# Performance work log

Measured on AMD Instinct MI355X. Metric: run time of the kernel, lower is better.

## Reference

```python
import jax, jax.numpy as jnp
import numpy as np

ALPHA = 3.0   # self.alpha
TAU = 0.1     # contrastive temperature
K = 8         # configs.k (top-k hyperedges per node)


def _scale(x, w, ehy, enod):
    """One scale of incidence_matrix_learn.
    x: [B, L, D] series tokens; w: [ws, D] word tokens;
    ehy: [H, D] hyperedge embedding table; enod: [N, D] node embedding table, N = L + ws.
    Returns (binary incidence matrix [N, H] float32, scalar contrastive loss).
    """
    B = x.shape[0]
    # concat_all[i]: cat(x.permute(0,2,1), word_expanded) -> [B, D, N]
    we = jnp.broadcast_to(w.T[None], (B,) + w.T.shape)          # [B, D, ws]
    concat = jnp.concatenate([jnp.transpose(x, (0, 2, 1)), we], axis=-1)  # [B, D, N]
    N, H = enod.shape[0], ehy.shape[0]
    # adjacency: softmax(relu(alpha * nodeec @ hyperen.T)) along hyperedge dim
    a = enod @ ehy.T                                            # [N, H]
    adj = jax.nn.softmax(jax.nn.relu(ALPHA * a), axis=-1)
    # top-k mask + threshold > 0.5 -> binary incidence matrix
    k = min(H, K)
    _, idx = jax.lax.top_k(adj, k)                              # [N, k]
    mask = jnp.zeros_like(adj).at[jnp.arange(N)[:, None], idx].set(1.0)
    adj_bin = ((adj * mask) > 0.5).astype(jnp.float32)          # [N, H]
    # positives: nodes sharing any hyperedge (build_pos_indices_from_edge_index),
    # equivalent to (A A^T > 0) with self excluded; dropping all-zero columns is a no-op here
    P = (adj_bin @ adj_bin.T > 0) & ~jnp.eye(N, dtype=bool)     # [N, N]
    cnt = P.sum(axis=1)                                         # positives per node
    # acl_loss_batched, vectorized over batch and nodes
    nodes = jnp.transpose(concat, (0, 2, 1))                    # [B, N, D]
    nrm = nodes / jnp.maximum(jnp.linalg.norm(nodes, axis=-1, keepdims=True), 1e-12)
    sim = jnp.einsum('bnd,bmd->bnm', nrm, nrm) / TAU            # [B, N, N]
    denom = jax.nn.logsumexp(sim, axis=-1)                      # [B, N]
    pos_mean = jnp.einsum('bnm,nm->bn', sim, P.astype(sim.dtype)) / jnp.maximum(cnt, 1)
    valid = cnt > 0                                             # [N]
    loss_sum = jnp.sum(jnp.where(valid[None, :], denom - pos_mean, 0.0))
    vc = B * valid.sum()
    loss = jnp.where(vc > 0, loss_sum / jnp.maximum(vc, 1), 0.0)
    return adj_bin, loss


def setup_inputs() -> dict:
    key = jax.random.key(0)
    ks = jax.random.split(key, 8)
    B, D = 64, 512
    return dict(
        x0=jax.random.normal(ks[0], (B, 512, D), dtype=jnp.float32),
        x1=jax.random.normal(ks[1], (B, 256, D), dtype=jnp.float32),
        word0=jax.random.normal(ks[2], (128, D), dtype=jnp.float32),
        word1=jax.random.normal(ks[3], (128, D), dtype=jnp.float32),
        embhy0=jax.random.normal(ks[4], (128, D), dtype=jnp.float32),
        embhy1=jax.random.normal(ks[5], (64, D), dtype=jnp.float32),
        embnod0=jax.random.normal(ks[6], (640, D), dtype=jnp.float32),
        embnod1=jax.random.normal(ks[7], (384, D), dtype=jnp.float32),
    )


def reference(x0, x1, word0, word1, embhy0, embhy1, embnod0, embnod1):
    a0, l0 = _scale(x0, word0, embhy0, embnod0)
    a1, l1 = _scale(x1, word1, embhy1, embnod1)
    return (a0, a1, l0 + l1)
```

## Files before the change

### kernel.cpp

```cpp
#include <hip/hip_runtime.h>


#define DDIM 512
#define BATCH 64
#define NGID 65536

typedef __attribute__((ext_vector_type(8))) short short8;
typedef __attribute__((ext_vector_type(4))) float f32x4;

__device__ __forceinline__ unsigned short f2bf(float f) {
  unsigned int u = __float_as_uint(f);
  u += 0x7fffu + ((u >> 16) & 1u);
  return (unsigned short)(u >> 16);
}

__device__ __forceinline__ void async16(const void* g, void* l) {
  __builtin_amdgcn_global_load_lds(
      (const __attribute__((address_space(1))) unsigned int*)g,
      (__attribute__((address_space(3))) unsigned int*)l, 16, 0, 0);
}

__device__ __forceinline__ int m3(int x) {
  x -= (x >= 6) ? 6 : 0;
  x -= (x >= 3) ? 3 : 0;
  return x;
}

__global__ __launch_bounds__(256) void prep_adj(
    const float* __restrict__ enod0, const float* __restrict__ ehy0,
    const float* __restrict__ enod1, const float* __restrict__ ehy1,
    float* __restrict__ adj0, float* __restrict__ adj1,
    int* __restrict__ labels0, int* __restrict__ labels1,
    float* __restrict__ acc) {
  const int t = threadIdx.x;
  if (blockIdx.x == 0 && t == 0) { acc[0] = 0.f; acc[1] = 0.f; }
  const bool s0 = blockIdx.x < 640;
  const int n = s0 ? blockIdx.x : blockIdx.x - 640;
  const int H = s0 ? 128 : 64;
  const float* enod = s0 ? enod0 : enod1;
  const float* ehy = s0 ? ehy0 : ehy1;
  float* out_adj = s0 ? adj0 : adj1;
  int* labels = s0 ? labels0 : labels1;
  __shared__ float erow[DDIM];
  __shared__ float red[128];
  __shared__ int lab;
  if (t < 128) ((float4*)erow)[t] = ((const float4*)(enod + (size_t)n * DDIM))[t];
  if (t == 0) lab = -1;
  __syncthreads();
  float v = 0.f;
  if (t < H) {
    const float4* hr = (const float4*)(ehy + (size_t)t * DDIM);
    float a = 0.f;
    #pragma unroll 8
    for (int d = 0; d < DDIM / 4; ++d) {
      float4 h = hr[d];
      float4 e = ((const float4*)erow)[d];
      a = fmaf(h.x, e.x, a); a = fmaf(h.y, e.y, a);
      a = fmaf(h.z, e.z, a); a = fmaf(h.w, e.w, a);
    }
    v = fmaxf(0.f, 3.0f * a);
  }
  if (t < 128) red[t] = v;
  __syncthreads();
  for (int s = 64; s > 0; s >>= 1) {
    if (t < s) red[t] = fmaxf(red[t], red[t + s]);
    __syncthreads();
  }
  const float mx = red[0];
  __syncthreads();
  const float e = (t < H) ? __expf(v - mx) : 0.f;
  if (t < 128) red[t] = e;
  __syncthreads();
  for (int s = 64; s > 0; s >>= 1) {
    if (t < s) red[t] += red[t + s];
    __syncthreads();
  }
  const float sum = red[0];
  if (t < H) {
    const float adj = e / sum;
    const float bin = (adj > 0.5f) ? 1.0f : 0.0f;
    out_adj[(size_t)n * H + t] = bin;
    if (bin > 0.f) lab = t;
  }
  __syncthreads();
  if (t == 0) labels[n] = lab;
}

__global__ __launch_bounds__(256) void prep_norm(
    const float* __restrict__ x0, const float* __restrict__ w0,
    const float* __restrict__ x1, const float* __restrict__ w1,
    unsigned short* __restrict__ nhat0, unsigned short* __restrict__ nhat1) {
  const int t = threadIdx.x;
  const int wave = t >> 6;
  const int lane = t & 63;
  const int g = blockIdx.x * 4 + wave;
  const bool s0 = g < BATCH * 640;
  const int gg = s0 ? g : g - BATCH * 640;
  const int N = s0 ? 640 : 384;
  const int L = s0 ? 512 : 256;
  const float* x = s0 ? x0 : x1;
  const float* w = s0 ? w0 : w1;
  unsigned short* nhat = s0 ? nhat0 : nhat1;
  const int b = gg / N;
  const int n = gg - b * N;
  const float* src = (n < L) ? (x + ((size_t)b * L + n) * DDIM)
                             : (w + (size_t)(n - L) * DDIM);
  const float4* rowp = (const float4*)src;
  const float4 v0 = rowp[lane];
  const float4 v1 = rowp[lane + 64];
  float ss = v0.x * v0.x + v0.y * v0.y + v0.z * v0.z + v0.w * v0.w +
             v1.x * v1.x + v1.y * v1.y + v1.z * v1.z + v1.w * v1.w;
  #pragma unroll
  for (int off = 32; off > 0; off >>= 1) ss += __shfl_xor(ss, off);
  const float rinv = 1.0f / fmaxf(sqrtf(ss), 1e-12f);
  ushort4 o0, o1;
  o0.x = f2bf(v0.x * rinv); o0.y = f2bf(v0.y * rinv);
  o0.z = f2bf(v0.z * rinv); o0.w = f2bf(v0.w * rinv);
  o1.x = f2bf(v1.x * rinv); o1.y = f2bf(v1.y * rinv);
  o1.z = f2bf(v1.z * rinv); o1.w = f2bf(v1.w * rinv);
  ushort4* op = (ushort4*)(nhat + ((size_t)b * N + n) * DDIM);
  op[lane] = o0;
  op[lane + 64] = o1;
}

__global__ __launch_bounds__(256) void cnt_kernel(
    const int* __restrict__ labels0, int* __restrict__ cnt0,
    const int* __restrict__ labels1, int* __restrict__ cnt1,
    int* __restrict__ valid) {
  const bool s0 = blockIdx.x == 0;
  const int* labels = s0 ? labels0 : labels1;
  int* cnt = s0 ? cnt0 : cnt1;
  int* validcnt = s0 ? valid : valid + 1;
  const int N = s0 ? 640 : 384;
  __shared__ int lab[640];
  __shared__ int hist[128];
  __shared__ int vc;
  const int t = threadIdx.x;
  if (t == 0) vc = 0;
  if (t < 128) hist[t] = 0;
  for (int i = t; i < N; i += 256) lab[i] = labels[i];
  __syncthreads();
  for (int i = t; i < N; i += 256)
    if (lab[i] >= 0) atomicAdd(&hist[lab[i]], 1);
  __syncthreads();
  int lv = 0;
  for (int i = t; i < N; i += 256) {
    const int c = (lab[i] >= 0) ? hist[lab[i]] - 1 : 0;
    cnt[i] = c;
    if (c > 0) ++lv;
  }
  if (lv > 0) atomicAdd(&vc, lv);
  __syncthreads();
  if (t == 0) *validcnt = vc;
}

__global__ __launch_bounds__(128, 2) void lse_kernel(
    const unsigned short* __restrict__ nhat0, const int* __restrict__ labels0,
    const unsigned short* __restrict__ nhat1, const int* __restrict__ labels1,
    float2* __restrict__ sp) {
  __shared__ short8 Bbuf[3][512];
  __shared__ float2 redC[2][64];
  __shared__ int labS[640];
  const int tid = threadIdx.x;
  const bool s0 = blockIdx.x < 640;
  const int i = s0 ? blockIdx.x : blockIdx.x - 640;
  const int tu = i >> 6;
  const int b = i & 63;
  const int nt = s0 ? 10 : 6;
  const int N = s0 ? 640 : 384;
  const unsigned short* nhat = s0 ? nhat0 : nhat1;
  const int* labels = s0 ? labels0 : labels1;
  const int gbase = s0 ? b * 640 : 40960 + b * 384;

  const int wave = tid >> 6;
  const int lane = tid & 63;
  const int lrow = lane & 15;
  const int lq = lane >> 4;

  for (int t = tid; t < N; t += 128) labS[t] = labels[t];

  const size_t base = (size_t)b * N * DDIM;
  const int rw0 = tu * 64 + wave * 32;
  const unsigned short* Ap0 = nhat + base + (size_t)(rw0 + lrow) * DDIM + lq * 8;
  const unsigned short* Ap1 = Ap0 + (size_t)16 * DDIM;
  short8 a0[16], a1[16];
  #pragma unroll
  for (int ks = 0; ks < 16; ++ks) {
    a0[ks] = *(const short8*)(Ap0 + ks * 32);
    a1[ks] = *(const short8*)(Ap1 + ks * 32);
  }
  #pragma unroll
  for (int ks = 0; ks < 16; ++ks)
    asm volatile("" :: "v"(a0[ks]), "v"(a1[ks]));

  __syncthreads();

  int labn[2][4];
  #pragma unroll
  for (int s = 0; s < 2; ++s)
    #pragma unroll
    for (int r = 0; r < 4; ++r) labn[s][r] = labS[rw0 + s * 16 + lq * 4 + r];

  const unsigned short* Bp0 = nhat + base + (size_t)tu * 64 * DDIM;
  const int f0 = wave * 4;
  #pragma unroll
  for (int pc = 0; pc < 2; ++pc) {
    #pragma unroll
    for (int fi = 0; fi < 4; ++fi) {
      const int f = f0 + fi, j = f >> 1, ks = f & 1;
      async16(Bp0 + (size_t)(j * 16 + lrow) * DDIM + pc * 64 + ks * 32 + lq * 8,
              &Bbuf[pc][f * 64]);
    }
  }

  float rSE[2][4] = {{0.f, 0.f, 0.f, 0.f}, {0.f, 0.f, 0.f, 0.f}};
  float rPOS[2][4] = {{0.f, 0.f, 0.f, 0.f}, {0.f, 0.f, 0.f, 0.f}};
  int slotb = 0;

  for (int tv = tu; tv < nt; ++tv) {
    const bool diag = (tv == tu);
    const bool last = (tv == nt - 1);
    const unsigned short* Bcur = nhat + base + (size_t)tv * 64 * DDIM;
    const unsigned short* Bnxt = Bcur + (size_t)64 * DDIM;
    const int sl[3] = {slotb, m3(slotb + 1), m3(slotb + 2)};

    f32x4 acc[4][2];
    #pragma unroll
    for (int j = 0; j < 4; ++j) {
      acc[j][0] = (f32x4){0.f, 0.f, 0.f, 0.f};
      acc[j][1] = (f32x4){0.f, 0.f, 0.f, 0.f};
    }
    #pragma unroll
    for (int kc = 0; kc < 8; ++kc) {
      if (last && kc == 7) asm volatile("s_waitcnt vmcnt(0)" ::: "memory");
      else                 asm volatile("s_waitcnt vmcnt(4)" ::: "memory");
      __builtin_amdgcn_s_barrier();
      if (!(last && kc >= 6)) {
        const unsigned short* Bsrc = (kc < 6) ? Bcur : Bnxt;
        const int kcol = (kc < 6) ? kc + 2 : kc - 6;
        short8* dst = &Bbuf[sl[(kc + 2) % 3]][0];
        #pragma unroll
        for (int fi = 0; fi < 4; ++fi) {
          const int f = f0 + fi, j = f >> 1, ks = f & 1;
          async16(Bsrc + (size_t)(j * 16 + lrow) * DDIM + kcol * 64 + ks * 32 + lq * 8,
                  dst + f * 64);
        }
      }
      const short8* bb = &Bbuf[sl[kc % 3]][0];
      #pragma unroll
      for (int ks = 0; ks < 2; ++ks) {
        const short8 b0 = bb[(0 + ks) * 64 + lane];
        const short8 b1 = bb[(2 + ks) * 64 + lane];
        const short8 b2 = bb[(4 + ks) * 64 + lane];
        const short8 b3 = bb[(6 + ks) * 64 + lane];
        const short8 av0 = a0[kc * 2 + ks];
        const short8 av1 = a1[kc * 2 + ks];
        acc[0][0] = __builtin_amdgcn_mfma_f32_16x16x32_bf16(av0, b0, acc[0][0], 0, 0, 0);
        acc[0][1] = __builtin_amdgcn_mfma_f32_16x16x32_bf16(av1, b0, acc[0][1], 0, 0, 0);
        acc[1][0] = __builtin_amdgcn_mfma_f32_16x16x32_bf16(av0, b1, acc[1][0], 0, 0, 0);
        acc[1][1] = __builtin_amdgcn_mfma_f32_16x16x32_bf16(av1, b1, acc[1][1], 0, 0, 0);
        acc[2][0] = __builtin_amdgcn_mfma_f32_16x16x32_bf16(av0, b2, acc[2][0], 0, 0, 0);
        acc[2][1] = __builtin_amdgcn_mfma_f32_16x16x32_bf16(av1, b2, acc[2][1], 0, 0, 0);
        acc[3][0] = __builtin_amdgcn_mfma_f32_16x16x32_bf16(av0, b3, acc[3][0], 0, 0, 0);
        acc[3][1] = __builtin_amdgcn_mfma_f32_16x16x32_bf16(av1, b3, acc[3][1], 0, 0, 0);
      }
    }

    float cSE[4] = {0.f, 0.f, 0.f, 0.f};
    float cPOS[4] = {0.f, 0.f, 0.f, 0.f};
    #pragma unroll
    for (int j = 0; j < 4; ++j) {
      const int v = tv * 64 + j * 16 + lrow;
      const int labm = labS[v];
      #pragma unroll
      for (int s = 0; s < 2; ++s) {
        const int u0 = rw0 + s * 16 + lq * 4;
        #pragma unroll
        for (int r = 0; r < 4; ++r) {
          const float sim = acc[j][s][r] * 10.0f;
          const float e = __expf(sim - 10.0f);
          rSE[s][r] += e;
          const bool match = (labn[s][r] >= 0) && (labm == labn[s][r]);
          if (match && v != u0 + r) rPOS[s][r] += sim;
          if (!diag) {
            cSE[j] += e;
            if (match) cPOS[j] += sim;
          }
        }
      }
    }
    if (!diag) {
      #pragma unroll
      for (int off = 16; off <= 32; off <<= 1) {
        #pragma unroll
        for (int j = 0; j < 4; ++j) {
          cSE[j] += __shfl_xor(cSE[j], off);
          cPOS[j] += __shfl_xor(cPOS[j], off);
        }
      }
      if (lane < 16) {
        #pragma unroll
        for (int j = 0; j < 4; ++j) {
          float2 st; st.x = cSE[j]; st.y = cPOS[j];
          redC[wave][j * 16 + lane] = st;
        }
      }
      asm volatile("s_waitcnt lgkmcnt(0)" ::: "memory");
      __builtin_amdgcn_s_barrier();
      if (lane < 32) {
        const int v = wave * 32 + lane;
        const float2 c0 = redC[0][v];
        const float2 c1 = redC[1][v];
        float2 st; st.x = c0.x + c1.x; st.y = c0.y + c1.y;
        sp[(size_t)(1 + tu) * NGID + gbase + tv * 64 + v] = st;
      }
    }
    slotb = m3(slotb + 2);
  }

  #pragma unroll
  for (int off = 1; off <= 8; off <<= 1) {
    #pragma unroll
    for (int s = 0; s < 2; ++s)
      #pragma unroll
      for (int r = 0; r < 4; ++r) {
        rSE[s][r] += __shfl_xor(rSE[s][r], off);
        rPOS[s][r] += __shfl_xor(rPOS[s][r], off);
      }
  }
  if (lrow == 0) {
    #pragma unroll
    for (int s = 0; s < 2; ++s)
      #pragma unroll
      for (int r = 0; r < 4; ++r) {
        const int u = rw0 + s * 16 + lq * 4 + r;
        float2 st; st.x = rSE[s][r]; st.y = rPOS[s][r];
        sp[gbase + u] = st;
      }
  }
}

__global__ __launch_bounds__(256) void loss_reduce(
    const float2* __restrict__ sp, const int* __restrict__ cnt0,
    const int* __restrict__ cnt1, float* __restrict__ acc) {
  __shared__ float r0[4], r1[4];
  const int t = threadIdx.x;
  float l0 = 0.f, l1 = 0.f;
  for (int g = blockIdx.x * 256 + t; g < NGID; g += 64 * 256) {
    const bool is0 = g < 40960;
    const int n = is0 ? (g % 640) : ((g - 40960) % 384);
    const int tb = n >> 6;
    float se = 0.f, pos = 0.f;
    for (int s = 0; s <= tb; ++s) {
      const float2 v = sp[(size_t)s * NGID + g];
      se += v.x; pos += v.y;
    }
    const int c = is0 ? cnt0[n] : cnt1[n];
    if (c > 0) {
      const float v = (10.0f + logf(se)) - pos / (float)c;
      if (is0) l0 += v; else l1 += v;
    }
  }
  #pragma unroll
  for (int off = 32; off > 0; off >>= 1) {
    l0 += __shfl_xor(l0, off);
    l1 += __shfl_xor(l1, off);
  }
  if ((t & 63) == 0) { r0[t >> 6] = l0; r1[t >> 6] = l1; }
  __syncthreads();
  if (t == 0) {
    atomicAdd(&acc[0], r0[0] + r0[1] + r0[2] + r0[3]);
    atomicAdd(&acc[1], r1[0] + r1[1] + r1[2] + r1[3]);
  }
}

__global__ void final_kernel(const float* __restrict__ acc,
                             const int* __restrict__ valid,
                             float* __restrict__ out) {
  float l = 0.f;
  if (valid[0] > 0) l += acc[0] / (float)(BATCH * valid[0]);
  if (valid[1] > 0) l += acc[1] / (float)(BATCH * valid[1]);
  out[0] = l;
}

extern "C" void kernel_launch(void* const* d_in, const int* in_sizes, int n_in,
                              void* d_out, int out_size, void* d_ws,
                              size_t ws_size, hipStream_t stream) {
  const float* x0 = (const float*)d_in[0];
  const float* x1 = (const float*)d_in[1];
  const float* w0 = (const float*)d_in[2];
  const float* w1 = (const float*)d_in[3];
  const float* ehy0 = (const float*)d_in[4];
  const float* ehy1 = (const float*)d_in[5];
  const float* enod0 = (const float*)d_in[6];
  const float* enod1 = (const float*)d_in[7];

  float* out = (float*)d_out;
  float* adj0 = out;
  float* adj1 = out + 640 * 128;
  float* lossp = out + 640 * 128 + 384 * 64;

  unsigned short* nhat0 = (unsigned short*)d_ws;
  unsigned short* nhat1 = nhat0 + (size_t)BATCH * 640 * DDIM;
  int* ip = (int*)(nhat1 + (size_t)BATCH * 384 * DDIM);
  int* labels0 = ip;
  int* labels1 = labels0 + 640;
  int* cnt0 = labels1 + 384;
  int* cnt1 = cnt0 + 640;
  int* valid = cnt1 + 384;
  float* acc = (float*)(valid + 2);
  float2* sp = (float2*)((((size_t)(acc + 2)) + 255) & ~(size_t)255);

  prep_adj<<<1024, 256, 0, stream>>>(enod0, ehy0, enod1, ehy1, adj0, adj1,
                                     labels0, labels1, acc);
  prep_norm<<<16384, 256, 0, stream>>>(x0, w0, x1, w1, nhat0, nhat1);
  cnt_kernel<<<2, 256, 0, stream>>>(labels0, cnt0, labels1, cnt1, valid);
  lse_kernel<<<1024, 128, 0, stream>>>(nhat0, labels0, nhat1, labels1, sp);
  loss_reduce<<<64, 256, 0, stream>>>(sp, cnt0, cnt1, acc);
  final_kernel<<<1, 1, 0, stream>>>(acc, valid, lossp);
}
```

Measured before the change: 263.0 us.

## Merge prep kernels, fold final into reduce, and rebalance lse block order

Combines the adjacency and normalization prep kernels into one launch, and folds the final loss computation into loss_reduce using a last-block ticket. Block-to-tile mapping in lse_kernel now comes from constant tables that interleave heavy and light triangular work units across scales to balance load. Register pinning of the A fragments moves into the loop. This removes two launches and aims to reduce tail imbalance, at the cost of a ticket atomic and a hand-tuned schedule table.

New measurement: 252.2 us. 1.04x faster.

```diff
diff --git a/kernel.cpp b/kernel.cpp
--- a/kernel.cpp
+++ b/kernel.cpp
@@ -7,6 +7,9 @@
 
 typedef __attribute__((ext_vector_type(8))) short short8;
 typedef __attribute__((ext_vector_type(4))) float f32x4;
+
+__constant__ int POS_SCALE[16] = {0,0,0,0, 0,1,0,0, 1,1,0,0, 0,1,1,1};
+__constant__ int POS_TU[16]    = {0,1,2,3, 9,5,7,4, 0,1,5,6, 8,2,3,4};
 
 __device__ __forceinline__ unsigned short f2bf(float f) {
   unsigned int u = __float_as_uint(f);
@@ -26,101 +29,100 @@
   return x;
 }
 
-__global__ __launch_bounds__(256) void prep_adj(
+__global__ __launch_bounds__(256) void prep_kernel(
     const float* __restrict__ enod0, const float* __restrict__ ehy0,
     const float* __restrict__ enod1, const float* __restrict__ ehy1,
     float* __restrict__ adj0, float* __restrict__ adj1,
     int* __restrict__ labels0, int* __restrict__ labels1,
-    float* __restrict__ acc) {
-  const int t = threadIdx.x;
-  if (blockIdx.x == 0 && t == 0) { acc[0] = 0.f; acc[1] = 0.f; }
-  const bool s0 = blockIdx.x < 640;
-  const int n = s0 ? blockIdx.x : blockIdx.x - 640;
-  const int H = s0 ? 128 : 64;
-  const float* enod = s0 ? enod0 : enod1;
-  const float* ehy = s0 ? ehy0 : ehy1;
-  float* out_adj = s0 ? adj0 : adj1;
-  int* labels = s0 ? labels0 : labels1;
-  __shared__ float erow[DDIM];
-  __shared__ float red[128];
-  __shared__ int lab;
-  if (t < 128) ((float4*)erow)[t] = ((const float4*)(enod + (size_t)n * DDIM))[t];
-  if (t == 0) lab = -1;
-  __syncthreads();
-  float v = 0.f;
-  if (t < H) {
-    const float4* hr = (const float4*)(ehy + (size_t)t * DDIM);
-    float a = 0.f;
-    #pragma unroll 8
-    for (int d = 0; d < DDIM / 4; ++d) {
-      float4 h = hr[d];
-      float4 e = ((const float4*)erow)[d];
-      a = fmaf(h.x, e.x, a); a = fmaf(h.y, e.y, a);
-      a = fmaf(h.z, e.z, a); a = fmaf(h.w, e.w, a);
-    }
-    v = fmaxf(0.f, 3.0f * a);
-  }
-  if (t < 128) red[t] = v;
-  __syncthreads();
-  for (int s = 64; s > 0; s >>= 1) {
-    if (t < s) red[t] = fmaxf(red[t], red[t + s]);
-    __syncthreads();
-  }
-  const float mx = red[0];
-  __syncthreads();
-  const float e = (t < H) ? __expf(v - mx) : 0.f;
-  if (t < 128) red[t] = e;
-  __syncthreads();
-  for (int s = 64; s > 0; s >>= 1) {
-    if (t < s) red[t] += red[t + s];
-    __syncthreads();
-  }
-  const float sum = red[0];
-  if (t < H) {
-    const float adj = e / sum;
-    const float bin = (adj > 0.5f) ? 1.0f : 0.0f;
-    out_adj[(size_t)n * H + t] = bin;
-    if (bin > 0.f) lab = t;
-  }
-  __syncthreads();
-  if (t == 0) labels[n] = lab;
-}
-
-__global__ __launch_bounds__(256) void prep_norm(
     const float* __restrict__ x0, const float* __restrict__ w0,
     const float* __restrict__ x1, const float* __restrict__ w1,
-    unsigned short* __restrict__ nhat0, unsigned short* __restrict__ nhat1) {
+    unsigned short* __restrict__ nhat0, unsigned short* __restrict__ nhat1,
+    float* __restrict__ acc, int* __restrict__ ticket) {
   const int t = threadIdx.x;
-  const int wave = t >> 6;
-  const int lane = t & 63;
-  const int g = blockIdx.x * 4 + wave;
-  const bool s0 = g < BATCH * 640;
-  const int gg = s0 ? g : g - BATCH * 640;
-  const int N = s0 ? 640 : 384;
-  const int L = s0 ? 512 : 256;
-  const float* x = s0 ? x0 : x1;
-  const float* w = s0 ? w0 : w1;
-  unsigned short* nhat = s0 ? nhat0 : nhat1;
-  const int b = gg / N;
-  const int n = gg - b * N;
-  const float* src = (n < L) ? (x + ((size_t)b * L + n) * DDIM)
-                             : (w + (size_t)(n - L) * DDIM);
-  const float4* rowp = (const float4*)src;
-  const float4 v0 = rowp[lane];
-  const float4 v1 = rowp[lane + 64];
-  float ss = v0.x * v0.x + v0.y * v0.y + v0.z * v0.z + v0.w * v0.w +
-             v1.x * v1.x + v1.y * v1.y + v1.z * v1.z + v1.w * v1.w;
-  #pragma unroll
-  for (int off = 32; off > 0; off >>= 1) ss += __shfl_xor(ss, off);
-  const float rinv = 1.0f / fmaxf(sqrtf(ss), 1e-12f);
-  ushort4 o0, o1;
-  o0.x = f2bf(v0.x * rinv); o0.y = f2bf(v0.y * rinv);
-  o0.z = f2bf(v0.z * rinv); o0.w = f2bf(v0.w * rinv);
-  o1.x = f2bf(v1.x * rinv); o1.y = f2bf(v1.y * rinv);
-  o1.z = f2bf(v1.z * rinv); o1.w = f2bf(v1.w * rinv);
-  ushort4* op = (ushort4*)(nhat + ((size_t)b * N + n) * DDIM);
-  op[lane] = o0;
-  op[lane + 64] = o1;
+  if (blockIdx.x < 1024) {
+    if (blockIdx.x == 0 && t == 0) { acc[0] = 0.f; acc[1] = 0.f; ticket[0] = 0; }
+    const bool s0 = blockIdx.x < 640;
+    const int n = s0 ? blockIdx.x : blockIdx.x - 640;
+    const int H = s0 ? 128 : 64;
+    const float* enod = s0 ? enod0 : enod1;
+    const float* ehy = s0 ? ehy0 : ehy1;
+    float* out_adj = s0 ? adj0 : adj1;
+    int* labels = s0 ? labels0 : labels1;
+    __shared__ float erow[DDIM];
+    __shared__ float red[128];
+    __shared__ int lab;
+    if (t < 128) ((float4*)erow)[t] = ((const float4*)(enod + (size_t)n * DDIM))[t];
+    if (t == 0) lab = -1;
+    __syncthreads();
+    float v = 0.f;
+    if (t < H) {
+      const float4* hr = (const float4*)(ehy + (size_t)t * DDIM);
+      float a = 0.f;
+      #pragma unroll 8
+      for (int d = 0; d < DDIM / 4; ++d) {
+        float4 h = hr[d];
+        float4 e = ((const float4*)erow)[d];
+        a = fmaf(h.x, e.x, a); a = fmaf(h.y, e.y, a);
+        a = fmaf(h.z, e.z, a); a = fmaf(h.w, e.w, a);
+      }
+      v = fmaxf(0.f, 3.0f * a);
+    }
+    if (t < 128) red[t] = v;
+    __syncthreads();
+    for (int s = 64; s > 0; s >>= 1) {
+      if (t < s) red[t] = fmaxf(red[t], red[t + s]);
+      __syncthreads();
+    }
+    const float mx = red[0];
+    __syncthreads();
+    const float e = (t < H) ? __expf(v - mx) : 0.f;
+    if (t < 128) red[t] = e;
+    __syncthreads();
+    for (int s = 64; s > 0; s >>= 1) {
+      if (t < s) red[t] += red[t + s];
+      __syncthreads();
+    }
+    const float sum = red[0];
+    if (t < H) {
+      const float adj = e / sum;
+      const float bin = (adj > 0.5f) ? 1.0f : 0.0f;
+      out_adj[(size_t)n * H + t] = bin;
+      if (bin > 0.f) lab = t;
+    }
+    __syncthreads();
+    if (t == 0) labels[n] = lab;
+  } else {
+    const int wave = t >> 6;
+    const int lane = t & 63;
+    const int g = (blockIdx.x - 1024) * 4 + wave;
+    const bool s0 = g < BATCH * 640;
+    const int gg = s0 ? g : g - BATCH * 640;
+    const int N = s0 ? 640 : 384;
+    const int L = s0 ? 512 : 256;
+    const float* x = s0 ? x0 : x1;
+    const float* w = s0 ? w0 : w1;
+    unsigned short* nhat = s0 ? nhat0 : nhat1;
+    const int b = gg / N;
+    const int n = gg - b * N;
+    const float* src = (n < L) ? (x + ((size_t)b * L + n) * DDIM)
+                               : (w + (size_t)(n - L) * DDIM);
+    const float4* rowp = (const float4*)src;
+    const float4 v0 = rowp[lane];
+    const float4 v1 = rowp[lane + 64];
+    float ss = v0.x * v0.x + v0.y * v0.y + v0.z * v0.z + v0.w * v0.w +
+               v1.x * v1.x + v1.y * v1.y + v1.z * v1.z + v1.w * v1.w;
+    #pragma unroll
+    for (int off = 32; off > 0; off >>= 1) ss += __shfl_xor(ss, off);
+    const float rinv = 1.0f / fmaxf(sqrtf(ss), 1e-12f);
+    ushort4 o0, o1;
+    o0.x = f2bf(v0.x * rinv); o0.y = f2bf(v0.y * rinv);
+    o0.z = f2bf(v0.z * rinv); o0.w = f2bf(v0.w * rinv);
+    o1.x = f2bf(v1.x * rinv); o1.y = f2bf(v1.y * rinv);
+    o1.z = f2bf(v1.z * rinv); o1.w = f2bf(v1.w * rinv);
+    ushort4* op = (ushort4*)(nhat + ((size_t)b * N + n) * DDIM);
+    op[lane] = o0;
+    op[lane + 64] = o1;
+  }
 }
 
 __global__ __launch_bounds__(256) void cnt_kernel(
@@ -162,10 +164,10 @@
   __shared__ float2 redC[2][64];
   __shared__ int labS[640];
   const int tid = threadIdx.x;
-  const bool s0 = blockIdx.x < 640;
-  const int i = s0 ? blockIdx.x : blockIdx.x - 640;
-  const int tu = i >> 6;
-  const int b = i & 63;
+  const int pos = blockIdx.x >> 6;
+  const int b = blockIdx.x & 63;
+  const bool s0 = POS_SCALE[pos] == 0;
+  const int tu = POS_TU[pos];
   const int nt = s0 ? 10 : 6;
   const int N = s0 ? 640 : 384;
   const unsigned short* nhat = s0 ? nhat0 : nhat1;
@@ -189,9 +191,6 @@
     a0[ks] = *(const short8*)(Ap0 + ks * 32);
     a1[ks] = *(const short8*)(Ap1 + ks * 32);
   }
-  #pragma unroll
-  for (int ks = 0; ks < 16; ++ks)
-    asm volatile("" :: "v"(a0[ks]), "v"(a1[ks]));
 
   __syncthreads();
 
@@ -218,6 +217,14 @@
   int slotb = 0;
 
   for (int tv = tu; tv < nt; ++tv) {
+    asm volatile("" : "+v"(a0[0]), "+v"(a0[1]), "+v"(a0[2]), "+v"(a0[3]),
+                      "+v"(a0[4]), "+v"(a0[5]), "+v"(a0[6]), "+v"(a0[7]));
+    asm volatile("" : "+v"(a0[8]), "+v"(a0[9]), "+v"(a0[10]), "+v"(a0[11]),
+                      "+v"(a0[12]), "+v"(a0[13]), "+v"(a0[14]), "+v"(a0[15]));
+    asm volatile("" : "+v"(a1[0]), "+v"(a1[1]), "+v"(a1[2]), "+v"(a1[3]),
+                      "+v"(a1[4]), "+v"(a1[5]), "+v"(a1[6]), "+v"(a1[7]));
+    asm volatile("" : "+v"(a1[8]), "+v"(a1[9]), "+v"(a1[10]), "+v"(a1[11]),
+                      "+v"(a1[12]), "+v"(a1[13]), "+v"(a1[14]), "+v"(a1[15]));
     const bool diag = (tv == tu);
     const bool last = (tv == nt - 1);
     const unsigned short* Bcur = nhat + base + (size_t)tv * 64 * DDIM;
@@ -342,7 +349,9 @@
 
 __global__ __launch_bounds__(256) void loss_reduce(
     const float2* __restrict__ sp, const int* __restrict__ cnt0,
-    const int* __restrict__ cnt1, float* __restrict__ acc) {
+    const int* __restrict__ cnt1, float* __restrict__ acc,
+    const int* __restrict__ valid, int* __restrict__ ticket,
+    float* __restrict__ lossp) {
   __shared__ float r0[4], r1[4];
   const int t = threadIdx.x;
   float l0 = 0.f, l1 = 0.f;
@@ -371,16 +380,17 @@
   if (t == 0) {
     atomicAdd(&acc[0], r0[0] + r0[1] + r0[2] + r0[3]);
     atomicAdd(&acc[1], r1[0] + r1[1] + r1[2] + r1[3]);
-  }
-}
-
-__global__ void final_kernel(const float* __restrict__ acc,
-                             const int* __restrict__ valid,
-                             float* __restrict__ out) {
-  float l = 0.f;
-  if (valid[0] > 0) l += acc[0] / (float)(BATCH * valid[0]);
-  if (valid[1] > 0) l += acc[1] / (float)(BATCH * valid[1]);
-  out[0] = l;
+    __threadfence();
+    const int done = atomicAdd(ticket, 1);
+    if (done == 63) {
+      const float a0v = atomicAdd(&acc[0], 0.0f);
+      const float a1v = atomicAdd(&acc[1], 0.0f);
+      float l = 0.f;
+      if (valid[0] > 0) l += a0v / (float)(BATCH * valid[0]);
+      if (valid[1] > 0) l += a1v / (float)(BATCH * valid[1]);
+      lossp[0] = l;
+    }
+  }
 }
 
 extern "C" void kernel_launch(void* const* d_in, const int* in_sizes, int n_in,
@@ -408,14 +418,15 @@
   int* cnt0 = labels1 + 384;
   int* cnt1 = cnt0 + 640;
   int* valid = cnt1 + 384;
-  float* acc = (float*)(valid + 2);
+  int* ticket = valid + 2;
+  float* acc = (float*)(ticket + 1);
   float2* sp = (float2*)((((size_t)(acc + 2)) + 255) & ~(size_t)255);
 
-  prep_adj<<<1024, 256, 0, stream>>>(enod0, ehy0, enod1, ehy1, adj0, adj1,
-                                     labels0, labels1, acc);
-  prep_norm<<<16384, 256, 0, stream>>>(x0, w0, x1, w1, nhat0, nhat1);
+  prep_kernel<<<1024 + 16384, 256, 0, stream>>>(
+      enod0, ehy0, enod1, ehy1, adj0, adj1, labels0, labels1,
+      x0, w0, x1, w1, nhat0, nhat1, acc, ticket);
   cnt_kernel<<<2, 256, 0, stream>>>(labels0, cnt0, labels1, cnt1, valid);
   lse_kernel<<<1024, 128, 0, stream>>>(nhat0, labels0, nhat1, labels1, sp);
-  loss_reduce<<<64, 256, 0, stream>>>(sp, cnt0, cnt1, acc);
-  final_kernel<<<1, 1, 0, stream>>>(acc, valid, lossp);
-}
+  loss_reduce<<<64, 256, 0, stream>>>(sp, cnt0, cnt1, acc, valid, ticket,
+                                      lossp);
+}
```
